# Kernel optimization log

Measured on AMD Instinct MI355X. Metric: run time of the kernel, lower is better.

The kernel has to match this reference:

```python
import jax, jax.numpy as jnp
import numpy as np

NEG_SLOPE = 0.2  # PyG GATConv default leaky_relu slope


def gat_conv(x_src, x_dst, src, dst, Ws, Wd, a_s, a_d, bias, n_dst, heads, ch,
             concat, edge_w=None, We=None, a_e=None):
    """PyG-style GATConv (bipartite, add_self_loops=False, eval mode)."""
    hs = (x_src @ Ws).reshape(-1, heads, ch)   # [Ns,H,C]
    hd = (x_dst @ Wd).reshape(-1, heads, ch)   # [Nd,H,C]
    a_src = jnp.einsum('nhc,hc->nh', hs, a_s)  # [Ns,H]
    a_dst = jnp.einsum('nhc,hc->nh', hd, a_d)  # [Nd,H]
    logits = a_src[src] + a_dst[dst]           # [E,H]
    if edge_w is not None:
        he = (edge_w[:, None] @ We).reshape(-1, heads, ch)  # lin_edge proj
        logits = logits + jnp.einsum('ehc,hc->eh', he, a_e)
    logits = jax.nn.leaky_relu(logits, NEG_SLOPE)
    # segment softmax grouped by destination node
    m = jax.ops.segment_max(logits, dst, num_segments=n_dst)
    e = jnp.exp(logits - m[dst])
    denom = jax.ops.segment_sum(e, dst, num_segments=n_dst)
    alpha = e / denom[dst]                     # [E,H]
    out = jax.ops.segment_sum(hs[src] * alpha[..., None], dst, num_segments=n_dst)
    out = out.reshape(n_dst, heads * ch) if concat else out.mean(axis=1)
    return out + bias


def setup_inputs() -> dict:
    key = jax.random.key(0)
    ks = jax.random.split(key, 40)
    NA = NB = 50000
    F = 128
    E = 800000
    HID = 100
    d = {}
    d['x_A'] = jax.random.normal(ks[0], (NA, F), jnp.float32)
    d['x_B'] = jax.random.normal(ks[1], (NB, F), jnp.float32)
    d['ei_AB'] = jax.random.randint(ks[2], (2, E), 0, NA)  # row0=src in A, row1=dst in B
    d['ei_BA'] = jax.random.randint(ks[3], (2, E), 0, NB)
    d['w_AB'] = jax.random.uniform(ks[4], (E,), jnp.float32)
    d['w_BA'] = jax.random.uniform(ks[5], (E,), jnp.float32)
    idx = [6]
    def p(shape):
        v = jax.random.normal(ks[idx[0]], shape, jnp.float32) * 0.1
        idx[0] += 1
        return v
    for et in ('AB', 'BA'):
        d['l1_%s_Ws' % et] = p((F, HID)); d['l1_%s_Wd' % et] = p((F, HID))
        d['l1_%s_as' % et] = p((4, 25)); d['l1_%s_ad' % et] = p((4, 25))
        d['l1_%s_We' % et] = p((1, HID)); d['l1_%s_ae' % et] = p((4, 25))
        d['l1_%s_b' % et] = p((HID,))
        d['l2_%s_Ws' % et] = p((HID, HID)); d['l2_%s_Wd' % et] = p((HID, HID))
        d['l2_%s_as' % et] = p((1, HID)); d['l2_%s_ad' % et] = p((1, HID))
        d['l2_%s_b' % et] = p((HID,))
    return d


def reference(x_A, x_B, ei_AB, ei_BA, w_AB, w_BA,
              l1_AB_Ws, l1_AB_Wd, l1_AB_as, l1_AB_ad, l1_AB_We, l1_AB_ae, l1_AB_b,
              l1_BA_Ws, l1_BA_Wd, l1_BA_as, l1_BA_ad, l1_BA_We, l1_BA_ae, l1_BA_b,
              l2_AB_Ws, l2_AB_Wd, l2_AB_as, l2_AB_ad, l2_AB_b,
              l2_BA_Ws, l2_BA_Wd, l2_BA_as, l2_BA_ad, l2_BA_b):
    NA, NB = x_A.shape[0], x_B.shape[0]
    s_ab, d_ab = ei_AB[0], ei_AB[1]
    s_ba, d_ba = ei_BA[0], ei_BA[1]
    # layer 1: heads=4, out=25 per head, concat -> 100, edge_dim=1
    hB = gat_conv(x_A, x_B, s_ab, d_ab, l1_AB_Ws, l1_AB_Wd, l1_AB_as, l1_AB_ad,
                  l1_AB_b, NB, 4, 25, True, w_AB, l1_AB_We, l1_AB_ae)
    hA = gat_conv(x_B, x_A, s_ba, d_ba, l1_BA_Ws, l1_BA_Wd, l1_BA_as, l1_BA_ad,
                  l1_BA_b, NA, 4, 25, True, w_BA, l1_BA_We, l1_BA_ae)
    # dropout is identity in eval mode
    hA = jax.nn.elu(hA)
    hB = jax.nn.elu(hB)
    # layer 2: heads=1, out=100, concat=False (mean over 1 head), no edge_dim
    oB = gat_conv(hA, hB, s_ab, d_ab, l2_AB_Ws, l2_AB_Wd, l2_AB_as, l2_AB_ad,
                  l2_AB_b, NB, 1, 100, False)
    oA = gat_conv(hB, hA, s_ba, d_ba, l2_BA_Ws, l2_BA_Wd, l2_BA_as, l2_BA_ad,
                  l2_BA_b, NA, 1, 100, False)
    return jnp.stack([oA, oB])  # [2, 50000, 100]
```

## Files before the change

### kernel.cpp

```cpp
#include <hip/hip_runtime.h>


#define NNODES 50000
#define NEDGES 800000
#define SCAN_T 1024
#define SCAN_NBLK ((NNODES + SCAN_T - 1) / SCAN_T)

typedef unsigned short u16;
typedef unsigned int u32;

__device__ __forceinline__ float b2f(u16 u) {
    union { u32 i; float f; } x;
    x.i = ((u32)u) << 16;
    return x.f;
}
__device__ __forceinline__ u16 f2b(float f) {
    union { float f; u32 i; } x;
    x.f = f;
    u32 r = x.i + 0x7FFFu + ((x.i >> 16) & 1u);
    return (u16)(r >> 16);
}

__global__ void ce_kernel(const float* __restrict__ WeA, const float* __restrict__ aeA,
                          const float* __restrict__ WeB, const float* __restrict__ aeB,
                          float* __restrict__ ce ) {
    const float* We = blockIdx.x ? WeB : WeA;
    const float* ae = blockIdx.x ? aeB : aeA;
    __shared__ float s[4];
    int tid = threadIdx.x;
    if (tid < 4) s[tid] = 0.f;
    __syncthreads();
    if (tid < 100) atomicAdd(&s[tid / 25], We[tid] * ae[tid]);
    __syncthreads();
    if (tid < 4) ce[blockIdx.x * 4 + tid] = s[tid];
}

__global__ void count_kernel(const int* __restrict__ eiA, const int* __restrict__ eiB,
                             int E, int* cntA, int* cntB) {
    int i = blockIdx.x * blockDim.x + threadIdx.x;
    if (i < E) atomicAdd(&cntA[eiA[E + i]], 1);
    else if (i < 2 * E) atomicAdd(&cntB[eiB[E + (i - E)]], 1);
}

__global__ __launch_bounds__(SCAN_T) void scanA_kernel(
    const int* __restrict__ cntA, const int* __restrict__ cntB,
    int* __restrict__ roA, int* __restrict__ roB, int* __restrict__ partial, int N) {
    const int dir = blockIdx.y;
    const int* cnt = dir ? cntB : cntA;
    int* ro = dir ? roB : roA;
    const int tid = threadIdx.x;
    const int i = blockIdx.x * SCAN_T + tid;
    __shared__ int sm[SCAN_T];
    sm[tid] = (i < N) ? cnt[i] : 0;
    __syncthreads();
    for (int off = 1; off < SCAN_T; off <<= 1) {
        int t = (tid >= off) ? sm[tid - off] : 0;
        __syncthreads();
        sm[tid] += t;
        __syncthreads();
    }
    if (i < N) ro[i + 1] = sm[tid];
    if (tid == SCAN_T - 1) partial[dir * 64 + blockIdx.x] = sm[tid];
}

__global__ void scanB_kernel(int* __restrict__ partial, int nblk) {
    __shared__ int sm[128];
    const int tid = threadIdx.x;
    sm[tid] = ((tid & 63) < nblk) ? partial[tid] : 0;
    __syncthreads();
    if (tid < 2) {
        int run = 0;
        for (int b = 0; b < nblk; ++b) {
            int t = sm[tid * 64 + b];
            sm[tid * 64 + b] = run;
            run += t;
        }
    }
    __syncthreads();
    partial[tid] = sm[tid];
}

__global__ __launch_bounds__(SCAN_T) void scanC_kernel(
    const int* __restrict__ cntA, const int* __restrict__ cntB,
    int* __restrict__ roA, int* __restrict__ roB,
    int* __restrict__ curA, int* __restrict__ curB,
    const int* __restrict__ partial, int N) {
    const int dir = blockIdx.y;
    const int* cnt = dir ? cntB : cntA;
    int* ro = dir ? roB : roA;
    int* cur = dir ? curB : curA;
    const int poff = partial[dir * 64 + blockIdx.x];
    const int i = blockIdx.x * SCAN_T + threadIdx.x;
    if (i < N) {
        int c = cnt[i];
        int r = ro[i + 1] + poff;
        ro[i + 1] = r;
        cur[i] = r - c;
        if (i == 0) ro[0] = 0;
    }
}

__global__ void fill_kernel(const int* __restrict__ eiA, const int* __restrict__ eiB,
                            const float* __restrict__ wA, const float* __restrict__ wB,
                            int E, int* curA, int* curB,
                            int* __restrict__ ssA, int* __restrict__ ssB,
                            float* __restrict__ swA, float* __restrict__ swB) {
    int i = blockIdx.x * blockDim.x + threadIdx.x;
    if (i < E) {
        int s = eiA[i], d = eiA[E + i];
        int pos = atomicAdd(&curA[d], 1);
        ssA[pos] = s; swA[pos] = wA[i];
    } else if (i < 2 * E) {
        int j = i - E;
        int s = eiB[j], d = eiB[E + j];
        int pos = atomicAdd(&curB[d], 1);
        ssB[pos] = s; swB[pos] = wB[j];
    }
}

struct GemmArgs {
    const float* X;
    const float* W;
    const float* a;
    void* H;
    float* att;
};

template <int K, int HEADS>
__global__ __launch_bounds__(256, 2) void gemm_att_kernel(
    GemmArgs g0, GemmArgs g1, GemmArgs g2, GemmArgs g3, int N) {
    const GemmArgs ga[4] = {g0, g1, g2, g3};
    const GemmArgs g = ga[blockIdx.y];
    constexpr int XS_STRIDE = 33;
    constexpr int XS_BUF = 128 * XS_STRIDE;
    constexpr int WS_STRIDE = 28;
    constexpr int WS_WAVE = 32 * WS_STRIDE;
    constexpr int WS_BUF = 4 * WS_WAVE;
    constexpr int SMEM_BYTES = (2 * XS_BUF + 2 * WS_BUF) * 4;
    __shared__ __align__(16) char smem[SMEM_BYTES];
    const int tid = threadIdx.x;
    const int lane = tid & 63;
    const int w = tid >> 6;
    const int node0 = blockIdx.x * 128;
    const int nA = node0 + lane;
    const int nB = node0 + 64 + lane;
    const bool vA = nA < N, vB = nB < N;

    const int c0 = __builtin_amdgcn_readfirstlane(25 * w);

    float acc0[25], acc1[25];
#pragma unroll
    for (int j = 0; j < 25; ++j) { acc0[j] = 0.f; acc1[j] = 0.f; }

    float* Xs = (float*)smem;
    float* Wsh = (float*)smem + 2 * XS_BUF;
    float4 rv[4];
    float wv[13];

    auto issue_x = [&](int k0) {
#pragma unroll
        for (int r = 0; r < 4; ++r) {
            const int s = tid + r * 256;
            const int n = s >> 3;
            const int ko = (s & 7) * 4;
            int row = node0 + n;
            if (row >= N) row = N - 1;
            const float* xp = g.X + (size_t)row * K + k0 + ko;
            if constexpr (K % 32 == 0) {
                rv[r] = *(const float4*)xp;
            } else {
                const int kb = k0 + ko;
                float4 v = make_float4(0.f, 0.f, 0.f, 0.f);
                if (kb + 3 < K) {
                    v = *(const float4*)xp;
                } else {
                    if (kb < K) v.x = xp[0];
                    if (kb + 1 < K) v.y = xp[1];
                    if (kb + 2 < K) v.z = xp[2];
                }
                rv[r] = v;
            }
        }
    };
    auto write_x = [&](int buf) {
#pragma unroll
        for (int r = 0; r < 4; ++r) {
            const int s = tid + r * 256;
            const int n = s >> 3;
            const int ko = (s & 7) * 4;
            float* dst = Xs + buf * XS_BUF + n * XS_STRIDE + ko;
            dst[0] = rv[r].x;
            dst[1] = rv[r].y;
            dst[2] = rv[r].z;
            dst[3] = rv[r].w;
        }
    };
    auto issue_w = [&](int k0, int kc) {
        const int lim = kc * 100;
#pragma unroll
        for (int r = 0; r < 13; ++r) {
            const int e = tid + r * 256;
            wv[r] = (e < lim) ? g.W[(size_t)k0 * 100 + e] : 0.f;
        }
    };
    auto write_w = [&](int buf, int kc) {
        const int lim = kc * 100;
#pragma unroll
        for (int r = 0; r < 13; ++r) {
            const int e = tid + r * 256;
            if (e < lim) {
                const int k = e / 100;
                const int j = e - k * 100;
                const int hd = j / 25;
                const int jj = j - hd * 25;
                Wsh[buf * WS_BUF + hd * WS_WAVE + k * WS_STRIDE + jj] = wv[r];
            }
        }
    };

    constexpr int C = (K + 31) / 32;
    {
        const int kc0 = (K < 32) ? K : 32;
        issue_x(0);
        issue_w(0, kc0);
        write_x(0);
        write_w(0, kc0);
    }
    __syncthreads();
    for (int c = 0; c < C; ++c) {
        const int k0 = c * 32;
        const int kc = (K - k0 < 32) ? (K - k0) : 32;
        const int kcn = (K - k0 - 32 < 32) ? (K - k0 - 32) : 32;
        if (c + 1 < C) {
            issue_x(k0 + 32);
            issue_w(k0 + 32, kcn);
        }
        const float* x0p = Xs + (c & 1) * XS_BUF + lane * XS_STRIDE;
        const float* x1p = x0p + 64 * XS_STRIDE;
        const float* wp = Wsh + (c & 1) * WS_BUF + w * WS_WAVE;
#pragma unroll 4
        for (int kk = 0; kk < kc; ++kk) {
            const float xs0 = x0p[kk];
            const float xs1 = x1p[kk];
            float wr[25];
#pragma unroll
            for (int j = 0; j < 25; ++j) wr[j] = wp[kk * WS_STRIDE + j];
#pragma unroll
            for (int j = 0; j < 25; ++j) {
                acc0[j] = fmaf(xs0, wr[j], acc0[j]);
                acc1[j] = fmaf(xs1, wr[j], acc1[j]);
            }
        }
        if (c + 1 < C) {
            __syncthreads();
            write_x((c + 1) & 1);
            write_w((c + 1) & 1, kcn);
        }
        __syncthreads();
    }

    float ap0 = 0.f, ap1 = 0.f;
#pragma unroll
    for (int j = 0; j < 25; ++j) {
        const float av = g.a[c0 + j];
        ap0 = fmaf(acc0[j], av, ap0);
        ap1 = fmaf(acc1[j], av, ap1);
    }

    const int rem = N - node0;
    if (HEADS == 4) {
        if (g.H == nullptr) {
            if (vA) g.att[(size_t)nA * 4 + w] = ap0;
            if (vB) g.att[(size_t)nB * 4 + w] = ap1;
        } else {
            u16* sh = (u16*)smem;
            u32* sh32 = (u32*)smem;
#pragma unroll
            for (int j = 0; j < 25; ++j) sh[lane * 106 + c0 + j] = f2b(acc0[j]);
            sh[lane * 106 + 100 + w] = f2b(ap0);
            __syncthreads();
            {
                const int limA = ((rem < 64) ? rem : 64) * 52;
                u32* Hb = (u32*)g.H + (size_t)node0 * 52;
                for (int i = tid; i < 64 * 52; i += 256) {
                    if (i < limA) {
                        int nd = i / 52;
                        Hb[i] = sh32[nd * 53 + (i - nd * 52)];
                    }
                }
            }
            __syncthreads();
#pragma unroll
            for (int j = 0; j < 25; ++j) sh[lane * 106 + c0 + j] = f2b(acc1[j]);
            sh[lane * 106 + 100 + w] = f2b(ap1);
            __syncthreads();
            {
                const int remB = rem - 64;
                const int limB = ((remB < 64) ? (remB < 0 ? 0 : remB) : 64) * 52;
                u32* Hb = (u32*)g.H + (size_t)(node0 + 64) * 52;
                for (int i = tid; i < 64 * 52; i += 256) {
                    if (i < limB) {
                        int nd = i / 52;
                        Hb[i] = sh32[nd * 53 + (i - nd * 52)];
                    }
                }
            }
        }
    } else {
        u16* sh = (u16*)smem;
        u32* sh32 = (u32*)smem;
        float* attp = (float*)(smem + 64 * 102 * 2);
        attp[w * 128 + lane] = ap0;
        attp[w * 128 + 64 + lane] = ap1;
        if (g.H != nullptr) {
#pragma unroll
            for (int j = 0; j < 25; ++j) sh[lane * 102 + c0 + j] = f2b(acc0[j]);
            __syncthreads();
            {
                const int limA = ((rem < 64) ? rem : 64) * 50;
                u32* Hb = (u32*)g.H + (size_t)node0 * 50;
                for (int i = tid; i < 64 * 50; i += 256) {
                    if (i < limA) {
                        int nd = i / 50;
                        Hb[i] = sh32[nd * 51 + (i - nd * 50)];
                    }
                }
                if (tid < 128 && node0 + tid < N)
                    g.att[node0 + tid] =
                        attp[tid] + attp[128 + tid] + attp[256 + tid] + attp[384 + tid];
            }
            __syncthreads();
#pragma unroll
            for (int j = 0; j < 25; ++j) sh[lane * 102 + c0 + j] = f2b(acc1[j]);
            __syncthreads();
            {
                const int remB = rem - 64;
                const int limB = ((remB < 64) ? (remB < 0 ? 0 : remB) : 64) * 50;
                u32* Hb = (u32*)g.H + (size_t)(node0 + 64) * 50;
                for (int i = tid; i < 64 * 50; i += 256) {
                    if (i < limB) {
                        int nd = i / 50;
                        Hb[i] = sh32[nd * 51 + (i - nd * 50)];
                    }
                }
            }
        } else {
            __syncthreads();
            if (tid < 128 && node0 + tid < N)
                g.att[node0 + tid] =
                    attp[tid] + attp[128 + tid] + attp[256 + tid] + attp[384 + tid];
        }
    }
}

struct Gather4Args {
    const int* ro;
    const int* ss;
    const float* sw;
    const u16* hp;
    const float* ad;
    const float* ce;
    const float* bias;
    float* outp;
};

__global__ __launch_bounds__(256) void gather4_kernel(Gather4Args ga0, Gather4Args ga1, int Nd) {
    const Gather4Args ga[2] = {ga0, ga1};
    const Gather4Args g = ga[blockIdx.y];
    int wid = (int)((blockIdx.x * blockDim.x + threadIdx.x) >> 6);
    if (wid >= Nd) return;
    const int n = __builtin_amdgcn_readfirstlane(wid);
    const int lane = threadIdx.x & 63;
    const int beg = g.ro[n], end = g.ro[n + 1];
    const bool act = (lane < 50);
    const int cc0 = act ? 2 * lane : 0;
    const int h0 = cc0 / 25;
    const int h1 = (cc0 + 1) / 25;
    const int aoff = 2 * (h0 >> 1);
    const float ce0 = g.ce[h0], ce1 = g.ce[h1];
    const float ad0 = g.ad[n * 4 + h0], ad1 = g.ad[n * 4 + h1];
    float acc0 = 0.f, acc1 = 0.f, d0 = 0.f, d1 = 0.f;

    auto edge = [&](u32 va, u32 aa, float wq, float& p0o, float& p1o) {
        const float as0 = b2f((h0 & 1) ? (u16)(aa >> 16) : (u16)aa);
        const float as1 = b2f((h1 & 1) ? (u16)(aa >> 16) : (u16)aa);
        float l0 = as0 + ad0 + wq * ce0;
        float l1 = as1 + ad1 + wq * ce1;
        l0 = fmaxf(l0, 0.2f * l0);
        l1 = fmaxf(l1, 0.2f * l1);
        const float p0 = __expf(l0);
        const float p1 = __expf(l1);
        acc0 = fmaf(p0, b2f((u16)va), acc0);
        acc1 = fmaf(p1, b2f((u16)(va >> 16)), acc1);
        p0o = p0;
        p1o = p1;
    };

    struct G4 { u32 va0, aa0, va1, aa1, va2, aa2, va3, aa3; float w0, w1, w2, w3; };
    auto load4 = [&](int off) -> G4 {
        G4 r;
        const int o = __builtin_amdgcn_readfirstlane(off);
        const int s0 = g.ss[o];
        const int s1 = g.ss[o + 1];
        const int s2 = g.ss[o + 2];
        const int s3 = g.ss[o + 3];
        r.w0 = g.sw[o];
        r.w1 = g.sw[o + 1];
        r.w2 = g.sw[o + 2];
        r.w3 = g.sw[o + 3];
        const u16* r0 = g.hp + (size_t)s0 * 104;
        const u16* r1 = g.hp + (size_t)s1 * 104;
        const u16* r2 = g.hp + (size_t)s2 * 104;
        const u16* r3 = g.hp + (size_t)s3 * 104;
        r.va0 = *(const u32*)(r0 + cc0);
        r.aa0 = *(const u32*)(r0 + 100 + aoff);
        r.va1 = *(const u32*)(r1 + cc0);
        r.aa1 = *(const u32*)(r1 + 100 + aoff);
        r.va2 = *(const u32*)(r2 + cc0);
        r.aa2 = *(const u32*)(r2 + 100 + aoff);
        r.va3 = *(const u32*)(r3 + cc0);
        r.aa3 = *(const u32*)(r3 + 100 + aoff);
        return r;
    };
    auto compute4 = [&](const G4& e) {
        float pa0, pa1, pb0, pb1;
        edge(e.va0, e.aa0, e.w0, pa0, pa1);
        edge(e.va1, e.aa1, e.w1, pb0, pb1);
        d0 += pa0 + pb0;
        d1 += pa1 + pb1;
        edge(e.va2, e.aa2, e.w2, pa0, pa1);
        edge(e.va3, e.aa3, e.w3, pb0, pb1);
        d0 += pa0 + pb0;
        d1 += pa1 + pb1;
    };

    int i = beg;
    const int last4 = beg + ((end - beg) & ~3);
    if (i < last4) {
        G4 cur = load4(i);
        i += 4;
        for (; i < last4; i += 4) {
            G4 nxt = load4(i);
            __builtin_amdgcn_sched_barrier(0);
            compute4(cur);
            cur = nxt;
        }
        compute4(cur);
    }
    if (i + 1 < end) {
        const int o = __builtin_amdgcn_readfirstlane(i);
        const int s0 = g.ss[o], s1 = g.ss[o + 1];
        const float w0 = g.sw[o], w1 = g.sw[o + 1];
        const u16* r0 = g.hp + (size_t)s0 * 104;
        const u16* r1 = g.hp + (size_t)s1 * 104;
        const u32 va0 = *(const u32*)(r0 + cc0);
        const u32 aa0 = *(const u32*)(r0 + 100 + aoff);
        const u32 va1 = *(const u32*)(r1 + cc0);
        const u32 aa1 = *(const u32*)(r1 + 100 + aoff);
        float pa0, pa1, pb0, pb1;
        edge(va0, aa0, w0, pa0, pa1);
        edge(va1, aa1, w1, pb0, pb1);
        d0 += pa0 + pb0;
        d1 += pa1 + pb1;
        i += 2;
    }
    if (i < end) {
        const int o = __builtin_amdgcn_readfirstlane(i);
        const int s0 = g.ss[o];
        const float w0 = g.sw[o];
        const u16* r0 = g.hp + (size_t)s0 * 104;
        const u32 va0 = *(const u32*)(r0 + cc0);
        const u32 aa0 = *(const u32*)(r0 + 100 + aoff);
        float pa0, pa1;
        edge(va0, aa0, w0, pa0, pa1);
        d0 += pa0;
        d1 += pa1;
    }

    if (act) {
        float r0 = (end > beg) ? acc0 / d0 : 0.f;
        float r1 = (end > beg) ? acc1 / d1 : 0.f;
        r0 += g.bias[cc0];
        r0 = (r0 > 0.f) ? r0 : (__expf(r0) - 1.f);
        r1 += g.bias[cc0 + 1];
        r1 = (r1 > 0.f) ? r1 : (__expf(r1) - 1.f);
        *(float2*)(g.outp + (size_t)n * 100 + cc0) = make_float2(r0, r1);
    }
}

struct Gather1Args {
    const int* ro;
    const int* ss;
    const u16* hp;
    const float* as_;
    const float* ad;
    const float* bias;
    float* outp;
};

__global__ __launch_bounds__(256) void gather1_kernel(Gather1Args ga0, Gather1Args ga1, int Nd) {
    const Gather1Args ga[2] = {ga0, ga1};
    const Gather1Args g = ga[blockIdx.y];
    int wid = (int)((blockIdx.x * blockDim.x + threadIdx.x) >> 6);
    if (wid >= Nd) return;
    const int n = __builtin_amdgcn_readfirstlane(wid);
    const int lane = threadIdx.x & 63;
    const int beg = g.ro[n], end = g.ro[n + 1];
    const bool act = (lane < 50);
    const int cc0 = act ? 2 * lane : 0;
    const float adn = g.ad[n];
    float acc0 = 0.f, acc1 = 0.f, d0 = 0.f;

    auto edge = [&](u32 va, float asq, float& po) {
        float l = asq + adn;
        l = fmaxf(l, 0.2f * l);
        const float p = __expf(l);
        acc0 = fmaf(p, b2f((u16)va), acc0);
        acc1 = fmaf(p, b2f((u16)(va >> 16)), acc1);
        po = p;
    };

    struct G1 { u32 va0, va1, va2, va3; float a0, a1, a2, a3; };
    auto load4 = [&](int off) -> G1 {
        G1 r;
        const int o = __builtin_amdgcn_readfirstlane(off);
        const int s0 = g.ss[o];
        const int s1 = g.ss[o + 1];
        const int s2 = g.ss[o + 2];
        const int s3 = g.ss[o + 3];
        r.a0 = g.as_[s0];
        r.a1 = g.as_[s1];
        r.a2 = g.as_[s2];
        r.a3 = g.as_[s3];
        r.va0 = *(const u32*)(g.hp + (size_t)s0 * 100 + cc0);
        r.va1 = *(const u32*)(g.hp + (size_t)s1 * 100 + cc0);
        r.va2 = *(const u32*)(g.hp + (size_t)s2 * 100 + cc0);
        r.va3 = *(const u32*)(g.hp + (size_t)s3 * 100 + cc0);
        return r;
    };
    auto compute4 = [&](const G1& e) {
        float pa, pb;
        edge(e.va0, e.a0, pa);
        edge(e.va1, e.a1, pb);
        d0 += pa + pb;
        edge(e.va2, e.a2, pa);
        edge(e.va3, e.a3, pb);
        d0 += pa + pb;
    };

    int i = beg;
    const int last4 = beg + ((end - beg) & ~3);
    if (i < last4) {
        G1 cur = load4(i);
        i += 4;
        for (; i < last4; i += 4) {
            G1 nxt = load4(i);
            __builtin_amdgcn_sched_barrier(0);
            compute4(cur);
            cur = nxt;
        }
        compute4(cur);
    }
    if (i + 1 < end) {
        const int o = __builtin_amdgcn_readfirstlane(i);
        const int s0 = g.ss[o], s1 = g.ss[o + 1];
        const float a0 = g.as_[s0], a1 = g.as_[s1];
        const u32 va0 = *(const u32*)(g.hp + (size_t)s0 * 100 + cc0);
        const u32 va1 = *(const u32*)(g.hp + (size_t)s1 * 100 + cc0);
        float pa, pb;
        edge(va0, a0, pa);
        edge(va1, a1, pb);
        d0 += pa + pb;
        i += 2;
    }
    if (i < end) {
        const int o = __builtin_amdgcn_readfirstlane(i);
        const int s0 = g.ss[o];
        const float a0 = g.as_[s0];
        const u32 va0 = *(const u32*)(g.hp + (size_t)s0 * 100 + cc0);
        float pa;
        edge(va0, a0, pa);
        d0 += pa;
    }

    if (act) {
        float r0 = (end > beg) ? acc0 / d0 : 0.f;
        float r1 = (end > beg) ? acc1 / d0 : 0.f;
        r0 += g.bias[cc0];
        r1 += g.bias[cc0 + 1];
        *(float2*)(g.outp + (size_t)n * 100 + cc0) = make_float2(r0, r1);
    }
}

extern "C" void kernel_launch(void* const* d_in, const int* in_sizes, int n_in,
                              void* d_out, int out_size, void* d_ws, size_t ws_size,
                              hipStream_t stream) {
    const float* x_A   = (const float*)d_in[0];
    const float* x_B   = (const float*)d_in[1];
    const int*   ei_AB = (const int*)d_in[2];
    const int*   ei_BA = (const int*)d_in[3];
    const float* w_AB  = (const float*)d_in[4];
    const float* w_BA  = (const float*)d_in[5];
    const float* l1AB_Ws = (const float*)d_in[6];
    const float* l1AB_Wd = (const float*)d_in[7];
    const float* l1AB_as = (const float*)d_in[8];
    const float* l1AB_ad = (const float*)d_in[9];
    const float* l1AB_We = (const float*)d_in[10];
    const float* l1AB_ae = (const float*)d_in[11];
    const float* l1AB_b  = (const float*)d_in[12];
    const float* l2AB_Ws = (const float*)d_in[13];
    const float* l2AB_Wd = (const float*)d_in[14];
    const float* l2AB_as = (const float*)d_in[15];
    const float* l2AB_ad = (const float*)d_in[16];
    const float* l2AB_b  = (const float*)d_in[17];
    const float* l1BA_Ws = (const float*)d_in[18];
    const float* l1BA_Wd = (const float*)d_in[19];
    const float* l1BA_as = (const float*)d_in[20];
    const float* l1BA_ad = (const float*)d_in[21];
    const float* l1BA_We = (const float*)d_in[22];
    const float* l1BA_ae = (const float*)d_in[23];
    const float* l1BA_b  = (const float*)d_in[24];
    const float* l2BA_Ws = (const float*)d_in[25];
    const float* l2BA_Wd = (const float*)d_in[26];
    const float* l2BA_as = (const float*)d_in[27];
    const float* l2BA_ad = (const float*)d_in[28];
    const float* l2BA_b  = (const float*)d_in[29];

    const int N = NNODES, E = NEDGES;

    size_t o = 0;
    auto alloc = [&](size_t n) { size_t r = o; o += (n + 63) & ~(size_t)63; return r; };
    size_t cntA = alloc(N), cntB = alloc(N);
    size_t roA = alloc(N + 1), roB = alloc(N + 1);
    size_t curA = alloc(N), curB = alloc(N);
    size_t ssA = alloc(E), ssB = alloc(E);
    size_t swA = alloc(E), swB = alloc(E);
    size_t ce8 = alloc(8);
    size_t part = alloc(128);
    size_t pHAB = alloc((size_t)N * 52);
    size_t pHBA = alloc((size_t)N * 52);
    size_t ad1B = alloc((size_t)N * 4), ad1A = alloc((size_t)N * 4);
    size_t hA1 = alloc((size_t)N * 100), hB1 = alloc((size_t)N * 100);
    size_t H2AB = alloc((size_t)N * 50);
    size_t H2BA = alloc((size_t)N * 50);
    size_t as2AB = alloc(N), as2BA = alloc(N);
    size_t ad2AB = alloc(N), ad2BA = alloc(N);
    (void)ws_size;

    float* wsf = (float*)d_ws;
    int*   wsi = (int*)d_ws;
    u32*   wsu = (u32*)d_ws;

    hipMemsetAsync(wsi + cntA, 0, sizeof(int) * (cntB + N - cntA), stream);

    ce_kernel<<<2, 128, 0, stream>>>(l1AB_We, l1AB_ae, l1BA_We, l1BA_ae, wsf + ce8);

    const int eb = (2 * E + 255) / 256;
    count_kernel<<<eb, 256, 0, stream>>>(ei_AB, ei_BA, E, wsi + cntA, wsi + cntB);
    scanA_kernel<<<dim3(SCAN_NBLK, 2), SCAN_T, 0, stream>>>(
        wsi + cntA, wsi + cntB, wsi + roA, wsi + roB, wsi + part, N);
    scanB_kernel<<<1, 128, 0, stream>>>(wsi + part, SCAN_NBLK);
    scanC_kernel<<<dim3(SCAN_NBLK, 2), SCAN_T, 0, stream>>>(
        wsi + cntA, wsi + cntB, wsi + roA, wsi + roB, wsi + curA, wsi + curB, wsi + part, N);
    fill_kernel<<<eb, 256, 0, stream>>>(ei_AB, ei_BA, w_AB, w_BA, E, wsi + curA, wsi + curB,
                                        wsi + ssA, wsi + ssB, wsf + swA, wsf + swB);

    const int gb = (N + 127) / 128;
    {
        GemmArgs g0 = {x_A, l1AB_Ws, l1AB_as, (void*)(wsu + pHAB), nullptr};
        GemmArgs g1 = {x_B, l1AB_Wd, l1AB_ad, nullptr, wsf + ad1B};
        GemmArgs g2 = {x_B, l1BA_Ws, l1BA_as, (void*)(wsu + pHBA), nullptr};
        GemmArgs g3 = {x_A, l1BA_Wd, l1BA_ad, nullptr, wsf + ad1A};
        gemm_att_kernel<128, 4><<<dim3(gb, 4), 256, 0, stream>>>(g0, g1, g2, g3, N);
    }

    const int wb = (N + 3) / 4;
    {
        Gather4Args g0 = {wsi + roA, wsi + ssA, wsf + swA, (const u16*)(wsu + pHAB),
                          wsf + ad1B, wsf + ce8, l1AB_b, wsf + hB1};
        Gather4Args g1 = {wsi + roB, wsi + ssB, wsf + swB, (const u16*)(wsu + pHBA),
                          wsf + ad1A, wsf + ce8 + 4, l1BA_b, wsf + hA1};
        gather4_kernel<<<dim3(wb, 2), 256, 0, stream>>>(g0, g1, N);
    }

    {
        GemmArgs g0 = {wsf + hA1, l2AB_Ws, l2AB_as, (void*)(wsu + H2AB), wsf + as2AB};
        GemmArgs g1 = {wsf + hB1, l2AB_Wd, l2AB_ad, nullptr, wsf + ad2AB};
        GemmArgs g2 = {wsf + hB1, l2BA_Ws, l2BA_as, (void*)(wsu + H2BA), wsf + as2BA};
        GemmArgs g3 = {wsf + hA1, l2BA_Wd, l2BA_ad, nullptr, wsf + ad2BA};
        gemm_att_kernel<100, 1><<<dim3(gb, 4), 256, 0, stream>>>(g0, g1, g2, g3, N);
    }

    float* out = (float*)d_out;
    {
        Gather1Args g0 = {wsi + roA, wsi + ssA, (const u16*)(wsu + H2AB), wsf + as2AB,
                          wsf + ad2AB, l2AB_b, out + (size_t)N * 100};
        Gather1Args g1 = {wsi + roB, wsi + ssB, (const u16*)(wsu + H2BA), wsf + as2BA,
                          wsf + ad2BA, l2BA_b, out};
        gather1_kernel<<<dim3(wb, 2), 256, 0, stream>>>(g0, g1, N);
    }
}
```

Baseline: 951.6 us.

## Pad bf16 feature rows to 256-byte stride and deepen gather prefetch

Projected bf16 source-feature rows are now stored with a 128-element (256-byte) stride instead of 104 or 100 elements, so each gathered row starts on an aligned boundary and touches fewer cache lines. The edge-gather loops also prefetch two groups of four edges ahead instead of one, to hide more memory latency. In exchange the workspace grows and more registers are live, which may reduce occupancy.

Result: faster. 921.2 us (-3.2%).

```diff
diff --git a/kernel.cpp b/kernel.cpp
--- a/kernel.cpp
+++ b/kernel.cpp
@@ -281,11 +281,12 @@
             __syncthreads();
             {
                 const int limA = ((rem < 64) ? rem : 64) * 52;
-                u32* Hb = (u32*)g.H + (size_t)node0 * 52;
+                u32* Hb = (u32*)g.H + (size_t)node0 * 64;
                 for (int i = tid; i < 64 * 52; i += 256) {
                     if (i < limA) {
                         int nd = i / 52;
-                        Hb[i] = sh32[nd * 53 + (i - nd * 52)];
+                        int off = i - nd * 52;
+                        Hb[nd * 64 + off] = sh32[nd * 53 + off];
                     }
                 }
             }
@@ -297,11 +298,12 @@
             {
                 const int remB = rem - 64;
                 const int limB = ((remB < 64) ? (remB < 0 ? 0 : remB) : 64) * 52;
-                u32* Hb = (u32*)g.H + (size_t)(node0 + 64) * 52;
+                u32* Hb = (u32*)g.H + (size_t)(node0 + 64) * 64;
                 for (int i = tid; i < 64 * 52; i += 256) {
                     if (i < limB) {
                         int nd = i / 52;
-                        Hb[i] = sh32[nd * 53 + (i - nd * 52)];
+                        int off = i - nd * 52;
+                        Hb[nd * 64 + off] = sh32[nd * 53 + off];
                     }
                 }
             }
@@ -318,11 +320,12 @@
             __syncthreads();
             {
                 const int limA = ((rem < 64) ? rem : 64) * 50;
-                u32* Hb = (u32*)g.H + (size_t)node0 * 50;
+                u32* Hb = (u32*)g.H + (size_t)node0 * 64;
                 for (int i = tid; i < 64 * 50; i += 256) {
                     if (i < limA) {
                         int nd = i / 50;
-                        Hb[i] = sh32[nd * 51 + (i - nd * 50)];
+                        int off = i - nd * 50;
+                        Hb[nd * 64 + off] = sh32[nd * 51 + off];
                     }
                 }
                 if (tid < 128 && node0 + tid < N)
@@ -336,11 +339,12 @@
             {
                 const int remB = rem - 64;
                 const int limB = ((remB < 64) ? (remB < 0 ? 0 : remB) : 64) * 50;
-                u32* Hb = (u32*)g.H + (size_t)(node0 + 64) * 50;
+                u32* Hb = (u32*)g.H + (size_t)(node0 + 64) * 64;
                 for (int i = tid; i < 64 * 50; i += 256) {
                     if (i < limB) {
                         int nd = i / 50;
-                        Hb[i] = sh32[nd * 51 + (i - nd * 50)];
+                        int off = i - nd * 50;
+                        Hb[nd * 64 + off] = sh32[nd * 51 + off];
                     }
                 }
             }
@@ -408,10 +412,10 @@
         r.w1 = g.sw[o + 1];
         r.w2 = g.sw[o + 2];
         r.w3 = g.sw[o + 3];
-        const u16* r0 = g.hp + (size_t)s0 * 104;
-        const u16* r1 = g.hp + (size_t)s1 * 104;
-        const u16* r2 = g.hp + (size_t)s2 * 104;
-        const u16* r3 = g.hp + (size_t)s3 * 104;
+        const u16* r0 = g.hp + (size_t)s0 * 128;
+        const u16* r1 = g.hp + (size_t)s1 * 128;
+        const u16* r2 = g.hp + (size_t)s2 * 128;
+        const u16* r3 = g.hp + (size_t)s3 * 128;
         r.va0 = *(const u32*)(r0 + cc0);
         r.aa0 = *(const u32*)(r0 + 100 + aoff);
         r.va1 = *(const u32*)(r1 + cc0);
@@ -436,23 +440,31 @@
 
     int i = beg;
     const int last4 = beg + ((end - beg) & ~3);
-    if (i < last4) {
+    const int ng = (last4 - beg) >> 2;
+    if (ng >= 2) {
         G4 cur = load4(i);
-        i += 4;
+        G4 nxt = load4(i + 4);
+        i += 8;
         for (; i < last4; i += 4) {
-            G4 nxt = load4(i);
+            G4 nn = load4(i);
             __builtin_amdgcn_sched_barrier(0);
             compute4(cur);
             cur = nxt;
+            nxt = nn;
         }
         compute4(cur);
+        compute4(nxt);
+    } else if (ng == 1) {
+        G4 cur = load4(i);
+        compute4(cur);
+        i += 4;
     }
     if (i + 1 < end) {
         const int o = __builtin_amdgcn_readfirstlane(i);
         const int s0 = g.ss[o], s1 = g.ss[o + 1];
         const float w0 = g.sw[o], w1 = g.sw[o + 1];
-        const u16* r0 = g.hp + (size_t)s0 * 104;
-        const u16* r1 = g.hp + (size_t)s1 * 104;
+        const u16* r0 = g.hp + (size_t)s0 * 128;
+        const u16* r1 = g.hp + (size_t)s1 * 128;
         const u32 va0 = *(const u32*)(r0 + cc0);
         const u32 aa0 = *(const u32*)(r0 + 100 + aoff);
         const u32 va1 = *(const u32*)(r1 + cc0);
@@ -468,7 +480,7 @@
         const int o = __builtin_amdgcn_readfirstlane(i);
         const int s0 = g.ss[o];
         const float w0 = g.sw[o];
-        const u16* r0 = g.hp + (size_t)s0 * 104;
+        const u16* r0 = g.hp + (size_t)s0 * 128;
         const u32 va0 = *(const u32*)(r0 + cc0);
         const u32 aa0 = *(const u32*)(r0 + 100 + aoff);
         float pa0, pa1;
@@ -532,10 +544,10 @@
         r.a1 = g.as_[s1];
         r.a2 = g.as_[s2];
         r.a3 = g.as_[s3];
-        r.va0 = *(const u32*)(g.hp + (size_t)s0 * 100 + cc0);
-        r.va1 = *(const u32*)(g.hp + (size_t)s1 * 100 + cc0);
-        r.va2 = *(const u32*)(g.hp + (size_t)s2 * 100 + cc0);
-        r.va3 = *(const u32*)(g.hp + (size_t)s3 * 100 + cc0);
+        r.va0 = *(const u32*)(g.hp + (size_t)s0 * 128 + cc0);
+        r.va1 = *(const u32*)(g.hp + (size_t)s1 * 128 + cc0);
+        r.va2 = *(const u32*)(g.hp + (size_t)s2 * 128 + cc0);
+        r.va3 = *(const u32*)(g.hp + (size_t)s3 * 128 + cc0);
         return r;
     };
     auto compute4 = [&](const G1& e) {
@@ -550,23 +562,31 @@
 
     int i = beg;
     const int last4 = beg + ((end - beg) & ~3);
-    if (i < last4) {
+    const int ng = (last4 - beg) >> 2;
+    if (ng >= 2) {
         G1 cur = load4(i);
-        i += 4;
+        G1 nxt = load4(i + 4);
+        i += 8;
         for (; i < last4; i += 4) {
-            G1 nxt = load4(i);
+            G1 nn = load4(i);
             __builtin_amdgcn_sched_barrier(0);
             compute4(cur);
             cur = nxt;
+            nxt = nn;
         }
         compute4(cur);
+        compute4(nxt);
+    } else if (ng == 1) {
+        G1 cur = load4(i);
+        compute4(cur);
+        i += 4;
     }
     if (i + 1 < end) {
         const int o = __builtin_amdgcn_readfirstlane(i);
         const int s0 = g.ss[o], s1 = g.ss[o + 1];
         const float a0 = g.as_[s0], a1 = g.as_[s1];
-        const u32 va0 = *(const u32*)(g.hp + (size_t)s0 * 100 + cc0);
-        const u32 va1 = *(const u32*)(g.hp + (size_t)s1 * 100 + cc0);
+        const u32 va0 = *(const u32*)(g.hp + (size_t)s0 * 128 + cc0);
+        const u32 va1 = *(const u32*)(g.hp + (size_t)s1 * 128 + cc0);
         float pa, pb;
         edge(va0, a0, pa);
         edge(va1, a1, pb);
@@ -577,7 +597,7 @@
         const int o = __builtin_amdgcn_readfirstlane(i);
         const int s0 = g.ss[o];
         const float a0 = g.as_[s0];
-        const u32 va0 = *(const u32*)(g.hp + (size_t)s0 * 100 + cc0);
+        const u32 va0 = *(const u32*)(g.hp + (size_t)s0 * 128 + cc0);
         float pa;
         edge(va0, a0, pa);
         d0 += pa;
@@ -637,12 +657,12 @@
     size_t swA = alloc(E), swB = alloc(E);
     size_t ce8 = alloc(8);
     size_t part = alloc(128);
-    size_t pHAB = alloc((size_t)N * 52);
-    size_t pHBA = alloc((size_t)N * 52);
+    size_t pHAB = alloc((size_t)N * 64);
+    size_t pHBA = alloc((size_t)N * 64);
     size_t ad1B = alloc((size_t)N * 4), ad1A = alloc((size_t)N * 4);
     size_t hA1 = alloc((size_t)N * 100), hB1 = alloc((size_t)N * 100);
-    size_t H2AB = alloc((size_t)N * 50);
-    size_t H2BA = alloc((size_t)N * 50);
+    size_t H2AB = alloc((size_t)N * 64);
+    size_t H2BA = alloc((size_t)N * 64);
     size_t as2AB = alloc(N), as2BA = alloc(N);
     size_t ad2AB = alloc(N), ad2BA = alloc(N);
     (void)ws_size;
```
